# Kernel optimization log

Hardware: AMD Instinct MI355X
Metric: run time of the kernel (lower is better)

## Reference

```python
import jax, jax.numpy as jnp
import numpy as np

B, BT = 64, 16              # total crops, true batch (B = 4 crops * BT)
IMG, PATCH, C = 224, 16, 3
EMB, HEADS, DEPTH = 192, 3, 12
MLP = 4 * EMB
NPATCH = (IMG // PATCH) ** 2      # 196
NTOK = NPATCH + 1                 # 197 (cls + patches)
NSLICE = 16
SAT_H, SAT_DK = 8, 32             # ScaledDotProductAttention(d_model=192, d_k=d_v=32, h=8)
SAT_D = SAT_H * SAT_DK            # 256


def setup_inputs() -> dict:
    ks = jax.random.split(jax.random.key(0), 16)
    n = lambda i, shape: jax.random.normal(ks[i], shape, jnp.float32) * 0.02
    z = lambda *s: jnp.zeros(s, jnp.float32)
    o = lambda *s: jnp.ones(s, jnp.float32)
    return {
        "x": jax.random.normal(ks[0], (B, C, IMG, IMG), jnp.float32),
        "x_g_norm": jax.random.uniform(ks[1], (BT, 1, IMG, IMG), dtype=jnp.float32),
        "per_li": jnp.linspace(1.0 / 16.0, 15.0 / 16.0, 15, dtype=jnp.float32),
        "per_li_var": jnp.linspace(0.01, 0.15, 15, dtype=jnp.float32),
        "patch_w": n(2, (EMB, C, PATCH, PATCH)), "patch_b": z(EMB),
        "cls_token": n(3, (1, 1, EMB)), "pos_embed": n(4, (1, NTOK, EMB)),
        "eleva_embed": n(5, (NSLICE, EMB)), "eleva_var_embed": n(6, (NSLICE, EMB)),
        "sat_wq": n(7, (EMB, SAT_D)), "sat_bq": z(SAT_D),
        "sat_wk": n(8, (EMB, SAT_D)), "sat_bk": z(SAT_D),
        "sat_wv": n(9, (EMB, SAT_D)), "sat_bv": z(SAT_D),
        "sat_wo": n(10, (SAT_D, EMB)), "sat_bo": z(EMB),
        "ln1_w": o(DEPTH, EMB), "ln1_b": z(DEPTH, EMB),
        "qkv_w": n(11, (DEPTH, EMB, 3 * EMB)),
        "proj_w": n(12, (DEPTH, EMB, EMB)), "proj_b": z(DEPTH, EMB),
        "ln2_w": o(DEPTH, EMB), "ln2_b": z(DEPTH, EMB),
        "fc1_w": n(13, (DEPTH, EMB, MLP)), "fc1_b": z(DEPTH, MLP),
        "fc2_w": n(14, (DEPTH, MLP, EMB)), "fc2_b": z(DEPTH, EMB),
        "lnf_w": o(EMB), "lnf_b": z(EMB),
    }


def _ln(x, w, b, eps=1e-5):
    mu = x.mean(-1, keepdims=True)
    var = ((x - mu) ** 2).mean(-1, keepdims=True)
    return (x - mu) * jax.lax.rsqrt(var + eps) * w + b


def reference(x, x_g_norm, per_li, per_li_var, patch_w, patch_b, cls_token, pos_embed,
              eleva_embed, eleva_var_embed, sat_wq, sat_bq, sat_wk, sat_bk, sat_wv, sat_bv,
              sat_wo, sat_bo, ln1_w, ln1_b, qkv_w, proj_w, proj_b, ln2_w, ln2_b,
              fc1_w, fc1_b, fc2_w, fc2_b, lnf_w, lnf_b):
    Btot, Bt = x.shape[0], x_g_norm.shape[0]
    # --- PatchEmbed (Conv2d patch=stride=16) ---
    feat = jax.lax.conv_general_dilated(
        x, patch_w, (PATCH, PATCH), 'VALID',
        dimension_numbers=('NCHW', 'OIHW', 'NCHW')) + patch_b[None, :, None, None]
    tok = feat.reshape(Btot, EMB, NPATCH).transpose(0, 2, 1)          # [B,196,E]
    tok = jnp.concatenate([jnp.broadcast_to(cls_token, (Btot, 1, EMB)), tok], 1)
    tok = tok + pos_embed                                             # [B,197,E]
    # --- elevation indices (bisect_left on per-sample mean / unbiased var) ---
    flat = x_g_norm.reshape(Bt, -1)
    idx = jnp.searchsorted(per_li, flat.mean(-1), side='left')
    vidx = jnp.searchsorted(per_li_var, jnp.var(flat, axis=-1, ddof=1), side='left')
    crops = Btot // Bt
    ele = jnp.tile(eleva_embed[idx], (crops, 1))                      # [B,E]
    vele = jnp.tile(eleva_var_embed[vidx], (crops, 1))                # [B,E]
    # --- tiny 3-token attention per (sample, token), batched ---
    at = jnp.stack([tok,
                    jnp.broadcast_to(ele[:, None, :], tok.shape),
                    jnp.broadcast_to(vele[:, None, :], tok.shape)], axis=2)  # [B,T,3,E]
    M = Btot * NTOK
    at = at.reshape(M, 3, EMB)
    q = (at @ sat_wq + sat_bq).reshape(M, 3, SAT_H, SAT_DK).transpose(0, 2, 1, 3)
    k = (at @ sat_wk + sat_bk).reshape(M, 3, SAT_H, SAT_DK).transpose(0, 2, 1, 3)
    v = (at @ sat_wv + sat_bv).reshape(M, 3, SAT_H, SAT_DK).transpose(0, 2, 1, 3)
    att = jax.nn.softmax(jnp.einsum('mhqd,mhkd->mhqk', q, k) / np.sqrt(SAT_DK).astype(np.float32), axis=-1)
    o = jnp.einsum('mhqk,mhkd->mhqd', att, v).transpose(0, 2, 1, 3).reshape(M, 3, SAT_D)
    o = o @ sat_wo + sat_bo                                           # [M,3,E]
    tok = o.sum(1).reshape(Btot, NTOK, EMB)   # token' + eleEm' + elevarEm'
    # --- standard ViT blocks ---
    hd = EMB // HEADS
    scale = hd ** -0.5
    for i in range(DEPTH):
        h = _ln(tok, ln1_w[i], ln1_b[i])
        qkv = (h @ qkv_w[i]).reshape(Btot, NTOK, 3, HEADS, hd).transpose(2, 0, 3, 1, 4)
        a = jax.nn.softmax(jnp.einsum('bhqd,bhkd->bhqk', qkv[0], qkv[1]) * scale, axis=-1)
        h = jnp.einsum('bhqk,bhkd->bhqd', a, qkv[2]).transpose(0, 2, 1, 3).reshape(Btot, NTOK, EMB)
        tok = tok + h @ proj_w[i] + proj_b[i]
        h2 = _ln(tok, ln2_w[i], ln2_b[i])
        h2 = jax.nn.gelu(h2 @ fc1_w[i] + fc1_b[i], approximate=False)
        tok = tok + h2 @ fc2_w[i] + fc2_b[i]
    tok = _ln(tok, lnf_w, lnf_b)
    return tok[:, 0]
```

## Files before the change

### kernel.cpp

```cpp
#include <hip/hip_runtime.h>
#include <hip/hip_bf16.h>
#include <math.h>

#define NB 64
#define NBT 16
#define IMG 224
#define CIN 3
#define EMB 192
#define NHEADS 3
#define DEPTH 12
#define MLPD (4*EMB)
#define NPATCH 196
#define NTOK 197
#define M_TOK (NB*NTOK)
#define M_PATCH (NB*NPATCH)
#define SAT_H 8
#define SAT_DK 32
#define SAT_D 256
#define KPV 232

typedef __attribute__((ext_vector_type(8))) short bf16x8;
typedef __attribute__((ext_vector_type(4))) float f32x4;
typedef __hip_bfloat16 bf16;

__device__ __forceinline__ float bf2f(ushort u) { return __uint_as_float(((unsigned)u) << 16); }
__device__ __forceinline__ ushort f2bf(float f) {
    bf16 h = __float2bfloat16(f);
    return *reinterpret_cast<ushort*>(&h);
}

__global__ __launch_bounds__(256) void stats_kernel(const float* __restrict__ xg,
    const float* __restrict__ per_li, const float* __restrict__ per_li_var,
    int* __restrict__ idx_out)
{
    int s = blockIdx.x;
    const float* row = xg + (size_t)s * (IMG*IMG);
    double lsum = 0.0, lsq = 0.0;
    for (int i = threadIdx.x; i < IMG*IMG; i += 256) {
        double v = (double)row[i]; lsum += v; lsq += v*v;
    }
    __shared__ double ssum[256], ssq[256];
    ssum[threadIdx.x] = lsum; ssq[threadIdx.x] = lsq;
    __syncthreads();
    for (int st = 128; st > 0; st >>= 1) {
        if (threadIdx.x < st) { ssum[threadIdx.x] += ssum[threadIdx.x+st]; ssq[threadIdx.x] += ssq[threadIdx.x+st]; }
        __syncthreads();
    }
    if (threadIdx.x == 0) {
        double n = (double)(IMG*IMG);
        double mean = ssum[0] / n;
        double var  = (ssq[0] - n*mean*mean) / (n - 1.0);
        int i1 = 0, i2 = 0;
        for (int j = 0; j < 15; j++) {
            if ((double)per_li[j] < mean) i1++;
            if ((double)per_li_var[j] < var) i2++;
        }
        idx_out[s] = i1; idx_out[16 + s] = i2;
    }
}

__global__ __launch_bounds__(256) void transpose_cast_kernel(const float* __restrict__ in,
    bf16* __restrict__ out, int K, int N)
{
    in  += (size_t)blockIdx.z*K*N;
    out += (size_t)blockIdx.z*N*K;
    __shared__ float t[32][33];
    int k0 = blockIdx.y*32, n0 = blockIdx.x*32;
    int tx = threadIdx.x & 31, ty = threadIdx.x >> 5;
    #pragma unroll
    for (int i = 0; i < 4; i++) {
        int k = ty + i*8;
        t[k][tx] = in[(size_t)(k0+k)*N + n0 + tx];
    }
    __syncthreads();
    #pragma unroll
    for (int i = 0; i < 4; i++) {
        int n = ty + i*8;
        out[(size_t)(n0+n)*K + k0 + tx] = __float2bfloat16(t[tx][n]);
    }
}

__global__ __launch_bounds__(256) void cast_kernel(const float* __restrict__ in, bf16* __restrict__ out, int n)
{
    int i = blockIdx.x*256 + threadIdx.x;
    if (i < n) out[i] = __float2bfloat16(in[i]);
}

__global__ __launch_bounds__(256) void im2col_kernel(const float* __restrict__ x, bf16* __restrict__ out)
{
    int e = blockIdx.x*256 + threadIdx.x;
    if (e >= M_PATCH*768) return;
    int row = e / 768, col = e % 768;
    int b = row / NPATCH, p = row % NPATCH;
    int py = p / 14, px = p % 14;
    int c = col >> 8, r8 = col & 255;
    int i = r8 >> 4, j = r8 & 15;
    out[e] = __float2bfloat16(x[(((size_t)b*CIN + c)*IMG + py*16 + i)*IMG + px*16 + j]);
}

__global__ void cls_kernel(const float* __restrict__ cls, const float* __restrict__ pos, bf16* __restrict__ tokb)
{
    int i = blockIdx.x*256 + threadIdx.x;
    if (i >= NB*EMB) return;
    int b = i / EMB, e = i % EMB;
    tokb[(size_t)(b*NTOK)*EMB + e] = __float2bfloat16(cls[e] + pos[e]);
}

template<int EPI, bool OBF>
__global__ __launch_bounds__(256) void mfma_gemm(
    const bf16* __restrict__ A, const bf16* __restrict__ Wt,
    const float* __restrict__ bias, const float* __restrict__ aux,
    void* __restrict__ Cv, int M, int N, int K, int ldc, float bias_scale)
{
    __shared__ bf16 As[64][72];
    __shared__ bf16 Bs[64][72];
    int tid = threadIdx.x;
    int wave = tid >> 6, lane = tid & 63;
    int wm = wave >> 1, wn = wave & 1;
    int m0 = blockIdx.y*64, n0 = blockIdx.x*64;
    f32x4 acc[2][2] = {};
    int sr = tid >> 3, sc = (tid & 7) * 8;

    for (int k0 = 0; k0 < K; k0 += 64) {
        #pragma unroll
        for (int it = 0; it < 2; it++) {
            int r = sr + it*32;
            *(uint4*)&As[r][sc] = *(const uint4*)(A  + (size_t)(m0 + r)*K + k0 + sc);
            *(uint4*)&Bs[r][sc] = *(const uint4*)(Wt + (size_t)(n0 + r)*K + k0 + sc);
        }
        __syncthreads();
        #pragma unroll
        for (int ks = 0; ks < 2; ks++) {
            int ko = ks*32 + (lane >> 4)*8;
            bf16x8 af[2], bfr[2];
            #pragma unroll
            for (int mi = 0; mi < 2; mi++) af[mi]  = *(const bf16x8*)&As[wm*32 + mi*16 + (lane & 15)][ko];
            #pragma unroll
            for (int ni = 0; ni < 2; ni++) bfr[ni] = *(const bf16x8*)&Bs[wn*32 + ni*16 + (lane & 15)][ko];
            #pragma unroll
            for (int mi = 0; mi < 2; mi++)
                #pragma unroll
                for (int ni = 0; ni < 2; ni++)
                    acc[mi][ni] = __builtin_amdgcn_mfma_f32_16x16x32_bf16(af[mi], bfr[ni], acc[mi][ni], 0, 0, 0);
        }
        __syncthreads();
    }
    #pragma unroll
    for (int mi = 0; mi < 2; mi++) {
        #pragma unroll
        for (int ni = 0; ni < 2; ni++) {
            int rbase = m0 + wm*32 + mi*16 + (lane >> 4)*4;
            int col   = n0 + wn*32 + ni*16 + (lane & 15);
            #pragma unroll
            for (int r = 0; r < 4; r++) {
                int row = rbase + r;
                float v = acc[mi][ni][r];
                if constexpr (EPI == 4) {
                    int b_ = row / NPATCH, p = row % NPATCH;
                    ((bf16*)Cv)[(size_t)(b_*NTOK + 1 + p)*EMB + col] =
                        __float2bfloat16(v + bias[col] + aux[(size_t)(1+p)*EMB + col]);
                } else if constexpr (EPI == 5) {
                    int hd = row >> 6, d = row & 63;
                    int bb = col / NTOK, t = col - bb*NTOK;
                    ((bf16*)Cv)[((size_t)((bb*3 + hd)*64 + d))*KPV + t] = __float2bfloat16(v);
                } else {
                    if constexpr (EPI == 1) v += bias[col]*bias_scale;
                    if constexpr (EPI == 2) v = ((float*)Cv)[(size_t)row*ldc + col] + v + bias[col];
                    if constexpr (EPI == 3) { v += bias[col]; v = 0.5f*v*(1.0f + erff(v*0.70710678118654752f)); }
                    if constexpr (OBF) ((bf16*)Cv)[(size_t)row*ldc + col] = __float2bfloat16(v);
                    else               ((float*)Cv)[(size_t)row*ldc + col] = v;
                }
            }
        }
    }
}

__global__ __launch_bounds__(256) void sat_rows_kernel(
    const float* __restrict__ eleva, const float* __restrict__ eleva_var,
    const float* __restrict__ wq, const float* __restrict__ bq,
    const float* __restrict__ wk, const float* __restrict__ bk,
    const float* __restrict__ wv, const float* __restrict__ bv,
    const int* __restrict__ idx, float* __restrict__ proj, float* __restrict__ sconst)
{
    int s = blockIdx.x;
    __shared__ float ev[2][EMB];
    __shared__ float pr[6][SAT_D];
    int t = threadIdx.x;
    for (int i = t; i < 2*EMB; i += 256) {
        if (i < EMB) ev[0][i] = eleva[(size_t)idx[s]*EMB + i];
        else         ev[1][i-EMB] = eleva_var[(size_t)idx[16+s]*EMB + (i-EMB)];
    }
    __syncthreads();
    for (int j = 0; j < 6; j++) {
        const float* vec = ev[(j >= 3) ? 1 : 0];
        const float* Wm = (j%3 == 0) ? wq : ((j%3 == 1) ? wk : wv);
        const float* bm = (j%3 == 0) ? bq : ((j%3 == 1) ? bk : bv);
        float accv = bm[t];
        for (int k = 0; k < EMB; k++) accv += vec[k]*Wm[(size_t)k*SAT_D + t];
        pr[j][t] = accv;
        proj[((size_t)s*6 + j)*SAT_D + t] = accv;
    }
    __syncthreads();
    if (t < 32) {
        int h = t >> 2, c = t & 3;
        const float* qv = pr[(c < 2) ? 0 : 3];
        const float* kv = pr[((c & 1) == 0) ? 1 : 4];
        float d = 0.f;
        for (int x = 0; x < SAT_DK; x++) d += qv[h*32+x]*kv[h*32+x];
        sconst[((size_t)s*8 + h)*4 + c] = d * 0.17677669529663687f;
    }
}

__global__ __launch_bounds__(256) void sat_attn_kernel(
    const bf16* __restrict__ qkv0, const float* __restrict__ proj,
    const float* __restrict__ sconst, bf16* __restrict__ osum)
{
    int b = blockIdx.x;
    int s = b & 15;
    __shared__ float pr[6][SAT_D];
    __shared__ float sc[8][4];
    for (int i = threadIdx.x; i < 6*SAT_D; i += 256) pr[i >> 8][i & 255] = proj[(size_t)s*6*SAT_D + i];
    if (threadIdx.x < 32) sc[threadIdx.x >> 2][threadIdx.x & 3] = sconst[(size_t)s*32 + threadIdx.x];
    __syncthreads();
    int t = threadIdx.x;
    if (t >= NTOK) return;
    size_t m = (size_t)b*NTOK + t;
    const ushort* q0 = (const ushort*)(qkv0 + m*768);
    const ushort* k0 = q0 + 256;
    const ushort* v0 = q0 + 512;
    const float inv = 0.17677669529663687f;
    for (int h = 0; h < SAT_H; h++) {
        int d0 = h*32;
        float S00=0,S01=0,S02=0,S10=0,S20=0;
        #pragma unroll 8
        for (int d = 0; d < 32; d++) {
            float qv = bf2f(q0[d0+d]), kv = bf2f(k0[d0+d]);
            S00 += qv*kv;
            S01 += qv*pr[1][d0+d];
            S02 += qv*pr[4][d0+d];
            S10 += pr[0][d0+d]*kv;
            S20 += pr[3][d0+d]*kv;
        }
        S00*=inv; S01*=inv; S02*=inv; S10*=inv; S20*=inv;
        float al=0.f, be=0.f, ga=0.f;
        {
            float mx = fmaxf(S00, fmaxf(S01, S02));
            float e0 = expf(S00-mx), e1 = expf(S01-mx), e2 = expf(S02-mx);
            float is = 1.0f/(e0+e1+e2); al += e0*is; be += e1*is; ga += e2*is;
        }
        {
            float a1 = sc[h][0], a2 = sc[h][1];
            float mx = fmaxf(S10, fmaxf(a1, a2));
            float e0 = expf(S10-mx), e1 = expf(a1-mx), e2 = expf(a2-mx);
            float is = 1.0f/(e0+e1+e2); al += e0*is; be += e1*is; ga += e2*is;
        }
        {
            float a1 = sc[h][2], a2 = sc[h][3];
            float mx = fmaxf(S20, fmaxf(a1, a2));
            float e0 = expf(S20-mx), e1 = expf(a1-mx), e2 = expf(a2-mx);
            float is = 1.0f/(e0+e1+e2); al += e0*is; be += e1*is; ga += e2*is;
        }
        #pragma unroll 8
        for (int d = 0; d < 32; d++)
            osum[m*SAT_D + d0 + d] = __float2bfloat16(al*bf2f(v0[d0+d]) + be*pr[2][d0+d] + ga*pr[5][d0+d]);
    }
}

__global__ __launch_bounds__(256) void vit_attn_mfma(
    const bf16* __restrict__ qkv, const bf16* __restrict__ vT, bf16* __restrict__ hout)
{
    __shared__ ushort Ks[208*72];
    __shared__ ushort Vt[64*KPV];
    __shared__ ushort Pl[4][16*KPV];

    int u = (blockIdx.x & 7)*96 + (blockIdx.x >> 3);
    int qg = u & 3, hd = (u >> 2) % 3, b = u / 12;
    int tid = threadIdx.x;
    size_t rowQ = (size_t)b*NTOK;

    for (int i = tid; i < 208*8; i += 256) {
        int k = i >> 3, c = i & 7;
        uint4 v = make_uint4(0u,0u,0u,0u);
        if (k < NTOK) v = *(const uint4*)(qkv + (rowQ + k)*384 + 192 + hd*64 + c*8);
        *(uint4*)&Ks[(size_t)k*72 + c*8] = v;
    }
    {
        const uint4* vsrc = (const uint4*)(vT + (size_t)((b*3 + hd)*64)*KPV);
        uint4* vdst = (uint4*)Vt;
        for (int i = tid; i < 64*KPV/8; i += 256) vdst[i] = vsrc[i];
    }
    __syncthreads();

    int wave = tid >> 6, lane = tid & 63;
    int qstart = (13*qg + 3) >> 2;
    int qcnt   = ((13*(qg+1) + 3) >> 2) - qstart;
    if (wave >= qcnt) return;
    int q0 = (qstart + wave)*16;
    int qcol = lane & 15, g = lane >> 4;

    bf16x8 qf[2] = {};
    if (q0 + qcol < NTOK) {
        const bf16* qp = qkv + (rowQ + q0 + qcol)*384 + hd*64 + g*8;
        qf[0] = *(const bf16x8*)qp;
        qf[1] = *(const bf16x8*)(qp + 32);
    }

    f32x4 st[13] = {};
    #pragma unroll
    for (int t = 0; t < 13; t++) {
        const ushort* krow = &Ks[(size_t)(16*t + qcol)*72];
        bf16x8 a0 = *(const bf16x8*)(krow + g*8);
        bf16x8 a1 = *(const bf16x8*)(krow + 32 + g*8);
        st[t] = __builtin_amdgcn_mfma_f32_16x16x32_bf16(a0, qf[0], st[t], 0, 0, 0);
        st[t] = __builtin_amdgcn_mfma_f32_16x16x32_bf16(a1, qf[1], st[t], 0, 0, 0);
    }

    const float scale = 0.125f;
    float mx = -1e30f;
    #pragma unroll
    for (int t = 0; t < 13; t++)
        #pragma unroll
        for (int r = 0; r < 4; r++) {
            int key = 16*t + 4*g + r;
            float s = st[t][r]*scale;
            st[t][r] = s;
            if (key < NTOK) mx = fmaxf(mx, s);
        }
    mx = fmaxf(mx, __shfl_xor(mx, 16));
    mx = fmaxf(mx, __shfl_xor(mx, 32));
    float sum = 0.f;
    #pragma unroll
    for (int t = 0; t < 13; t++)
        #pragma unroll
        for (int r = 0; r < 4; r++) {
            int key = 16*t + 4*g + r;
            float e = (key < NTOK) ? __expf(st[t][r] - mx) : 0.f;
            st[t][r] = e; sum += e;
        }
    sum += __shfl_xor(sum, 16);
    sum += __shfl_xor(sum, 32);
    float isv = 1.f/sum;

    ushort* P = Pl[wave];
    #pragma unroll
    for (int t = 0; t < 13; t++)
        #pragma unroll
        for (int r = 0; r < 4; r++)
            P[(size_t)qcol*KPV + 16*t + 4*g + r] = f2bf(st[t][r]*isv);
    #pragma unroll
    for (int r = 0; r < 4; r++)
        P[(size_t)qcol*KPV + 208 + 4*g + r] = 0;

    f32x4 oacc[4] = {};
    #pragma unroll
    for (int ks = 0; ks < 7; ks++) {
        bf16x8 pf = *(const bf16x8*)&P[(size_t)qcol*KPV + ks*32 + g*8];
        #pragma unroll
        for (int dt = 0; dt < 4; dt++) {
            bf16x8 vf = *(const bf16x8*)&Vt[(size_t)(dt*16 + qcol)*KPV + ks*32 + g*8];
            oacc[dt] = __builtin_amdgcn_mfma_f32_16x16x32_bf16(pf, vf, oacc[dt], 0, 0, 0);
        }
    }

    int nq = NTOK - q0; if (nq > 16) nq = 16;
    #pragma unroll
    for (int dt = 0; dt < 4; dt++)
        #pragma unroll
        for (int r = 0; r < 4; r++) {
            int q = 4*g + r;
            if (q < nq)
                hout[(rowQ + q0 + q)*EMB + hd*64 + dt*16 + qcol] = __float2bfloat16(oacc[dt][r]);
        }
}

__global__ __launch_bounds__(256) void ln_kernel(const float* __restrict__ in,
    const float* __restrict__ w, const float* __restrict__ b_, bf16* __restrict__ out, int nrows)
{
    int r = blockIdx.x*4 + (threadIdx.x >> 6);
    int lane = threadIdx.x & 63;
    if (r >= nrows) return;
    const float* x = in + (size_t)r*EMB;
    float x0 = x[lane], x1 = x[lane+64], x2 = x[lane+128];
    float s = x0+x1+x2;
    for (int o = 32; o > 0; o >>= 1) s += __shfl_xor(s, o);
    float mu = s * (1.0f/EMB);
    float d0 = x0-mu, d1 = x1-mu, d2 = x2-mu;
    float ss = d0*d0 + d1*d1 + d2*d2;
    for (int o = 32; o > 0; o >>= 1) ss += __shfl_xor(ss, o);
    float rs = rsqrtf(ss*(1.0f/EMB) + 1e-5f);
    bf16* y = out + (size_t)r*EMB;
    y[lane]     = __float2bfloat16(d0*rs*w[lane]     + b_[lane]);
    y[lane+64]  = __float2bfloat16(d1*rs*w[lane+64]  + b_[lane+64]);
    y[lane+128] = __float2bfloat16(d2*rs*w[lane+128] + b_[lane+128]);
}

__global__ __launch_bounds__(64) void final_ln_kernel(const float* __restrict__ tok,
    const float* __restrict__ w, const float* __restrict__ b_, float* __restrict__ out)
{
    int b = blockIdx.x, lane = threadIdx.x;
    const float* x = tok + (size_t)b*NTOK*EMB;
    float x0 = x[lane], x1 = x[lane+64], x2 = x[lane+128];
    float s = x0+x1+x2;
    for (int o = 32; o > 0; o >>= 1) s += __shfl_xor(s, o);
    float mu = s * (1.0f/EMB);
    float d0 = x0-mu, d1 = x1-mu, d2 = x2-mu;
    float ss = d0*d0 + d1*d1 + d2*d2;
    for (int o = 32; o > 0; o >>= 1) ss += __shfl_xor(ss, o);
    float rs = rsqrtf(ss*(1.0f/EMB) + 1e-5f);
    out[(size_t)b*EMB + lane]     = d0*rs*w[lane]     + b_[lane];
    out[(size_t)b*EMB + lane+64]  = d1*rs*w[lane+64]  + b_[lane+64];
    out[(size_t)b*EMB + lane+128] = d2*rs*w[lane+128] + b_[lane+128];
}

extern "C" void kernel_launch(void* const* d_in, const int* in_sizes, int n_in,
                              void* d_out, int out_size, void* d_ws, size_t ws_size,
                              hipStream_t stream)
{
    const float* x          = (const float*)d_in[0];
    const float* xg         = (const float*)d_in[1];
    const float* per_li     = (const float*)d_in[2];
    const float* per_li_var = (const float*)d_in[3];
    const float* patch_w    = (const float*)d_in[4];
    const float* patch_b    = (const float*)d_in[5];
    const float* cls_token  = (const float*)d_in[6];
    const float* pos_embed  = (const float*)d_in[7];
    const float* eleva      = (const float*)d_in[8];
    const float* eleva_var  = (const float*)d_in[9];
    const float* sat_wq     = (const float*)d_in[10];
    const float* sat_bq     = (const float*)d_in[11];
    const float* sat_wk     = (const float*)d_in[12];
    const float* sat_bk     = (const float*)d_in[13];
    const float* sat_wv     = (const float*)d_in[14];
    const float* sat_bv     = (const float*)d_in[15];
    const float* sat_wo     = (const float*)d_in[16];
    const float* sat_bo     = (const float*)d_in[17];
    const float* ln1_w      = (const float*)d_in[18];
    const float* ln1_b      = (const float*)d_in[19];
    const float* qkv_w      = (const float*)d_in[20];
    const float* proj_w     = (const float*)d_in[21];
    const float* proj_b     = (const float*)d_in[22];
    const float* ln2_w      = (const float*)d_in[23];
    const float* ln2_b      = (const float*)d_in[24];
    const float* fc1_w      = (const float*)d_in[25];
    const float* fc1_b      = (const float*)d_in[26];
    const float* fc2_w      = (const float*)d_in[27];
    const float* fc2_b      = (const float*)d_in[28];
    const float* lnf_w      = (const float*)d_in[29];
    const float* lnf_b      = (const float*)d_in[30];
    float* out = (float*)d_out;

    char* p = (char*)d_ws;
    float* tokf = (float*)p;                 p += (size_t)M_TOK*EMB*4;
    bf16* hb    = (bf16*)p;                  p += (size_t)M_TOK*EMB*2;
    bf16* tokb  = (bf16*)p;                  p += (size_t)M_TOK*EMB*2;
    bf16* qkvb  = (bf16*)p;                  p += (size_t)M_TOK*768*2;
    bf16* osum  = (bf16*)p;                  p += (size_t)M_TOK*SAT_D*2;
    bf16* vTb   = (bf16*)p;                  p += (size_t)NB*3*64*KPV*2;
    bf16* qkv_wt  = (bf16*)p;                p += (size_t)DEPTH*576*EMB*2;
    bf16* proj_wt = (bf16*)p;                p += (size_t)DEPTH*EMB*EMB*2;
    bf16* fc1_wt  = (bf16*)p;                p += (size_t)DEPTH*MLPD*EMB*2;
    bf16* fc2_wt  = (bf16*)p;                p += (size_t)DEPTH*EMB*MLPD*2;
    bf16* patch_wb= (bf16*)p;                p += (size_t)EMB*768*2;
    bf16* sat_wqt = (bf16*)p;                p += (size_t)SAT_D*EMB*2;
    bf16* sat_wkt = (bf16*)p;                p += (size_t)SAT_D*EMB*2;
    bf16* sat_wvt = (bf16*)p;                p += (size_t)SAT_D*EMB*2;
    bf16* sat_wot = (bf16*)p;                p += (size_t)EMB*SAT_D*2;
    float* projb  = (float*)p;               p += 16*6*SAT_D*4;
    float* sconst = (float*)p;               p += 16*32*4;
    int*   idxb   = (int*)p;

    transpose_cast_kernel<<<dim3(576/32, EMB/32, DEPTH), 256, 0, stream>>>(qkv_w,  qkv_wt,  EMB, 576);
    transpose_cast_kernel<<<dim3(EMB/32, EMB/32, DEPTH), 256, 0, stream>>>(proj_w, proj_wt, EMB, EMB);
    transpose_cast_kernel<<<dim3(MLPD/32, EMB/32, DEPTH), 256, 0, stream>>>(fc1_w, fc1_wt,  EMB, MLPD);
    transpose_cast_kernel<<<dim3(EMB/32, MLPD/32, DEPTH), 256, 0, stream>>>(fc2_w, fc2_wt,  MLPD, EMB);
    transpose_cast_kernel<<<dim3(SAT_D/32, EMB/32, 1), 256, 0, stream>>>(sat_wq, sat_wqt, EMB, SAT_D);
    transpose_cast_kernel<<<dim3(SAT_D/32, EMB/32, 1), 256, 0, stream>>>(sat_wk, sat_wkt, EMB, SAT_D);
    transpose_cast_kernel<<<dim3(SAT_D/32, EMB/32, 1), 256, 0, stream>>>(sat_wv, sat_wvt, EMB, SAT_D);
    transpose_cast_kernel<<<dim3(EMB/32, SAT_D/32, 1), 256, 0, stream>>>(sat_wo, sat_wot, SAT_D, EMB);
    cast_kernel<<<(EMB*768 + 255)/256, 256, 0, stream>>>(patch_w, patch_wb, EMB*768);

    stats_kernel<<<16, 256, 0, stream>>>(xg, per_li, per_li_var, idxb);
    im2col_kernel<<<(M_PATCH*768 + 255)/256, 256, 0, stream>>>(x, qkvb);
    mfma_gemm<4,true><<<dim3(EMB/64, M_PATCH/64), 256, 0, stream>>>(
        qkvb, patch_wb, patch_b, pos_embed, tokb, M_PATCH, EMB, 768, EMB, 1.0f);
    cls_kernel<<<(NB*EMB + 255)/256, 256, 0, stream>>>(cls_token, pos_embed, tokb);
    sat_rows_kernel<<<16, 256, 0, stream>>>(eleva, eleva_var, sat_wq, sat_bq, sat_wk, sat_bk,
                                            sat_wv, sat_bv, idxb, projb, sconst);
    mfma_gemm<1,true><<<dim3(SAT_D/64, M_TOK/64), 256, 0, stream>>>(
        tokb, sat_wqt, sat_bq, nullptr, qkvb + 0,   M_TOK, SAT_D, EMB, 768, 1.0f);
    mfma_gemm<1,true><<<dim3(SAT_D/64, M_TOK/64), 256, 0, stream>>>(
        tokb, sat_wkt, sat_bk, nullptr, qkvb + 256, M_TOK, SAT_D, EMB, 768, 1.0f);
    mfma_gemm<1,true><<<dim3(SAT_D/64, M_TOK/64), 256, 0, stream>>>(
        tokb, sat_wvt, sat_bv, nullptr, qkvb + 512, M_TOK, SAT_D, EMB, 768, 1.0f);
    sat_attn_kernel<<<NB, 256, 0, stream>>>(qkvb, projb, sconst, osum);
    mfma_gemm<1,false><<<dim3(EMB/64, M_TOK/64), 256, 0, stream>>>(
        osum, sat_wot, sat_bo, nullptr, tokf, M_TOK, EMB, SAT_D, EMB, 3.0f);
    for (int i = 0; i < DEPTH; i++) {
        ln_kernel<<<M_TOK/4, 256, 0, stream>>>(tokf, ln1_w + i*EMB, ln1_b + i*EMB, hb, M_TOK);
        mfma_gemm<0,true><<<dim3(384/64, M_TOK/64), 256, 0, stream>>>(
            hb, qkv_wt + (size_t)i*576*EMB, nullptr, nullptr, qkvb, M_TOK, 384, EMB, 384, 1.0f);
        mfma_gemm<5,true><<<dim3(M_TOK/64, EMB/64), 256, 0, stream>>>(
            qkv_wt + ((size_t)i*576 + 384)*EMB, hb, nullptr, nullptr, vTb, EMB, M_TOK, EMB, 0, 1.0f);
        vit_attn_mfma<<<768, 256, 0, stream>>>(qkvb, vTb, hb);
        mfma_gemm<2,false><<<dim3(EMB/64, M_TOK/64), 256, 0, stream>>>(
            hb, proj_wt + (size_t)i*EMB*EMB, proj_b + i*EMB, nullptr, tokf, M_TOK, EMB, EMB, EMB, 1.0f);
        ln_kernel<<<M_TOK/4, 256, 0, stream>>>(tokf, ln2_w + i*EMB, ln2_b + i*EMB, hb, M_TOK);
        mfma_gemm<3,true><<<dim3(MLPD/64, M_TOK/64), 256, 0, stream>>>(
            hb, fc1_wt + (size_t)i*MLPD*EMB, fc1_b + i*MLPD, nullptr, qkvb, M_TOK, MLPD, EMB, MLPD, 1.0f);
        mfma_gemm<2,false><<<dim3(EMB/64, M_TOK/64), 256, 0, stream>>>(
            qkvb, fc2_wt + (size_t)i*EMB*MLPD, fc2_b + i*EMB, nullptr, tokf, M_TOK, EMB, MLPD, EMB, 1.0f);
    }
    final_ln_kernel<<<NB, 64, 0, stream>>>(tokf, lnf_w, lnf_b, out);
}
```

Measured before the change: 1.636 ms.

## Fuse LayerNorm into full-row GEMM epilogues, merge SAT QKV GEMMs, split stats

```diff
diff --git a/kernel.cpp b/kernel.cpp
--- a/kernel.cpp
+++ b/kernel.cpp
@@ -29,34 +29,46 @@
     return *reinterpret_cast<ushort*>(&h);
 }
 
-__global__ __launch_bounds__(256) void stats_kernel(const float* __restrict__ xg,
-    const float* __restrict__ per_li, const float* __restrict__ per_li_var,
-    int* __restrict__ idx_out)
-{
-    int s = blockIdx.x;
-    const float* row = xg + (size_t)s * (IMG*IMG);
-    double lsum = 0.0, lsq = 0.0;
-    for (int i = threadIdx.x; i < IMG*IMG; i += 256) {
-        double v = (double)row[i]; lsum += v; lsq += v*v;
+__global__ __launch_bounds__(256) void stats1_kernel(const float* __restrict__ xg, double* __restrict__ part)
+{
+    int j = blockIdx.x, s = blockIdx.y;
+    const float4* src = (const float4*)(xg + (size_t)s*(IMG*IMG)) + (size_t)j*784;
+    double ls = 0.0, lq = 0.0;
+    for (int i = threadIdx.x; i < 784; i += 256) {
+        float4 v = src[i];
+        double a = v.x, b = v.y, c = v.z, d = v.w;
+        ls += a+b+c+d;
+        lq += a*a + b*b + c*c + d*d;
     }
     __shared__ double ssum[256], ssq[256];
-    ssum[threadIdx.x] = lsum; ssq[threadIdx.x] = lsq;
+    ssum[threadIdx.x] = ls; ssq[threadIdx.x] = lq;
     __syncthreads();
     for (int st = 128; st > 0; st >>= 1) {
         if (threadIdx.x < st) { ssum[threadIdx.x] += ssum[threadIdx.x+st]; ssq[threadIdx.x] += ssq[threadIdx.x+st]; }
         __syncthreads();
     }
     if (threadIdx.x == 0) {
-        double n = (double)(IMG*IMG);
-        double mean = ssum[0] / n;
-        double var  = (ssq[0] - n*mean*mean) / (n - 1.0);
-        int i1 = 0, i2 = 0;
-        for (int j = 0; j < 15; j++) {
-            if ((double)per_li[j] < mean) i1++;
-            if ((double)per_li_var[j] < var) i2++;
-        }
-        idx_out[s] = i1; idx_out[16 + s] = i2;
-    }
+        part[(size_t)(s*16 + j)*2]     = ssum[0];
+        part[(size_t)(s*16 + j)*2 + 1] = ssq[0];
+    }
+}
+
+__global__ __launch_bounds__(64) void stats2_kernel(const double* __restrict__ part,
+    const float* __restrict__ per_li, const float* __restrict__ per_li_var, int* __restrict__ idx_out)
+{
+    int s = blockIdx.x;
+    if (threadIdx.x != 0) return;
+    double sum = 0.0, sq = 0.0;
+    for (int j = 0; j < 16; j++) { sum += part[(size_t)(s*16+j)*2]; sq += part[(size_t)(s*16+j)*2+1]; }
+    double n = (double)(IMG*IMG);
+    double mean = sum / n;
+    double var  = (sq - n*mean*mean) / (n - 1.0);
+    int i1 = 0, i2 = 0;
+    for (int j = 0; j < 15; j++) {
+        if ((double)per_li[j] < mean) i1++;
+        if ((double)per_li_var[j] < var) i2++;
+    }
+    idx_out[s] = i1; idx_out[16 + s] = i2;
 }
 
 __global__ __launch_bounds__(256) void transpose_cast_kernel(const float* __restrict__ in,
@@ -84,6 +96,15 @@
 {
     int i = blockIdx.x*256 + threadIdx.x;
     if (i < n) out[i] = __float2bfloat16(in[i]);
+}
+
+__global__ __launch_bounds__(256) void concat3_kernel(const float* __restrict__ a,
+    const float* __restrict__ b, const float* __restrict__ c, float* __restrict__ o)
+{
+    int i = blockIdx.x*256 + threadIdx.x;
+    if (i < 256) o[i] = a[i];
+    else if (i < 512) o[i] = b[i-256];
+    else if (i < 768) o[i] = c[i-512];
 }
 
 __global__ __launch_bounds__(256) void im2col_kernel(const float* __restrict__ x, bf16* __restrict__ out)
@@ -171,6 +192,73 @@
                     else               ((float*)Cv)[(size_t)row*ldc + col] = v;
                 }
             }
+        }
+    }
+}
+
+template<bool RESID>
+__global__ __launch_bounds__(256) void mfma_gemm_ln(
+    const bf16* __restrict__ A, const bf16* __restrict__ Wt,
+    const float* __restrict__ bias, float bias_scale,
+    const float* __restrict__ lnw, const float* __restrict__ lnb,
+    float* __restrict__ tokf, bf16* __restrict__ hbB, int K)
+{
+    __shared__ bf16 As[64][72];
+    __shared__ bf16 Bs[192][72];
+    __shared__ float sB[192], sW[192], sLb[192];
+    int tid = threadIdx.x;
+    int m0 = blockIdx.x*64;
+    if (tid < 192) { sB[tid] = bias[tid]*bias_scale; sW[tid] = lnw[tid]; sLb[tid] = lnb[tid]; }
+    int wave = tid >> 6, lane = tid & 63;
+    int qc = lane & 15, g = lane >> 4;
+    f32x4 acc[12] = {};
+    int sr = tid >> 3, sc = (tid & 7)*8;
+
+    for (int k0 = 0; k0 < K; k0 += 64) {
+        #pragma unroll
+        for (int it = 0; it < 2; it++)
+            *(uint4*)&As[sr + it*32][sc] = *(const uint4*)(A + (size_t)(m0 + sr + it*32)*K + k0 + sc);
+        #pragma unroll
+        for (int it = 0; it < 6; it++)
+            *(uint4*)&Bs[sr + it*32][sc] = *(const uint4*)(Wt + (size_t)(sr + it*32)*K + k0 + sc);
+        __syncthreads();
+        #pragma unroll
+        for (int ks = 0; ks < 2; ks++) {
+            bf16x8 af = *(const bf16x8*)&As[wave*16 + qc][ks*32 + g*8];
+            #pragma unroll
+            for (int c = 0; c < 12; c++) {
+                bf16x8 bf_ = *(const bf16x8*)&Bs[c*16 + qc][ks*32 + g*8];
+                acc[c] = __builtin_amdgcn_mfma_f32_16x16x32_bf16(af, bf_, acc[c], 0, 0, 0);
+            }
+        }
+        __syncthreads();
+    }
+    #pragma unroll
+    for (int r = 0; r < 4; r++) {
+        int row = m0 + wave*16 + g*4 + r;
+        float v[12];
+        float s = 0.f;
+        #pragma unroll
+        for (int c = 0; c < 12; c++) {
+            int col = c*16 + qc;
+            float t = acc[c][r] + sB[col];
+            if constexpr (RESID) t += tokf[(size_t)row*EMB + col];
+            v[c] = t; s += t;
+        }
+        #pragma unroll
+        for (int o = 1; o < 16; o <<= 1) s += __shfl_xor(s, o);
+        float mu = s * (1.0f/EMB);
+        float ss = 0.f;
+        #pragma unroll
+        for (int c = 0; c < 12; c++) { float d = v[c]-mu; ss += d*d; }
+        #pragma unroll
+        for (int o = 1; o < 16; o <<= 1) ss += __shfl_xor(ss, o);
+        float rsn = rsqrtf(ss*(1.0f/EMB) + 1e-5f);
+        #pragma unroll
+        for (int c = 0; c < 12; c++) {
+            int col = c*16 + qc;
+            tokf[(size_t)row*EMB + col] = v[c];
+            hbB[(size_t)row*EMB + col] = __float2bfloat16((v[c]-mu)*rsn*sW[col] + sLb[col]);
         }
     }
 }
@@ -371,27 +459,6 @@
             if (q < nq)
                 hout[(rowQ + q0 + q)*EMB + hd*64 + dt*16 + qcol] = __float2bfloat16(oacc[dt][r]);
         }
-}
-
-__global__ __launch_bounds__(256) void ln_kernel(const float* __restrict__ in,
-    const float* __restrict__ w, const float* __restrict__ b_, bf16* __restrict__ out, int nrows)
-{
-    int r = blockIdx.x*4 + (threadIdx.x >> 6);
-    int lane = threadIdx.x & 63;
-    if (r >= nrows) return;
-    const float* x = in + (size_t)r*EMB;
-    float x0 = x[lane], x1 = x[lane+64], x2 = x[lane+128];
-    float s = x0+x1+x2;
-    for (int o = 32; o > 0; o >>= 1) s += __shfl_xor(s, o);
-    float mu = s * (1.0f/EMB);
-    float d0 = x0-mu, d1 = x1-mu, d2 = x2-mu;
-    float ss = d0*d0 + d1*d1 + d2*d2;
-    for (int o = 32; o > 0; o >>= 1) ss += __shfl_xor(ss, o);
-    float rs = rsqrtf(ss*(1.0f/EMB) + 1e-5f);
-    bf16* y = out + (size_t)r*EMB;
-    y[lane]     = __float2bfloat16(d0*rs*w[lane]     + b_[lane]);
-    y[lane+64]  = __float2bfloat16(d1*rs*w[lane+64]  + b_[lane+64]);
-    y[lane+128] = __float2bfloat16(d2*rs*w[lane+128] + b_[lane+128]);
 }
 
 __global__ __launch_bounds__(64) void final_ln_kernel(const float* __restrict__ tok,
@@ -461,54 +528,57 @@
     bf16* fc1_wt  = (bf16*)p;                p += (size_t)DEPTH*MLPD*EMB*2;
     bf16* fc2_wt  = (bf16*)p;                p += (size_t)DEPTH*EMB*MLPD*2;
     bf16* patch_wb= (bf16*)p;                p += (size_t)EMB*768*2;
-    bf16* sat_wqt = (bf16*)p;                p += (size_t)SAT_D*EMB*2;
-    bf16* sat_wkt = (bf16*)p;                p += (size_t)SAT_D*EMB*2;
-    bf16* sat_wvt = (bf16*)p;                p += (size_t)SAT_D*EMB*2;
+    bf16* sat_wqkvt = (bf16*)p;              p += (size_t)3*SAT_D*EMB*2;
     bf16* sat_wot = (bf16*)p;                p += (size_t)EMB*SAT_D*2;
+    float* sat_bqkv = (float*)p;             p += 768*4;
     float* projb  = (float*)p;               p += 16*6*SAT_D*4;
     float* sconst = (float*)p;               p += 16*32*4;
+    double* statp = (double*)p;              p += 256*2*8;
     int*   idxb   = (int*)p;
 
     transpose_cast_kernel<<<dim3(576/32, EMB/32, DEPTH), 256, 0, stream>>>(qkv_w,  qkv_wt,  EMB, 576);
     transpose_cast_kernel<<<dim3(EMB/32, EMB/32, DEPTH), 256, 0, stream>>>(proj_w, proj_wt, EMB, EMB);
     transpose_cast_kernel<<<dim3(MLPD/32, EMB/32, DEPTH), 256, 0, stream>>>(fc1_w, fc1_wt,  EMB, MLPD);
     transpose_cast_kernel<<<dim3(EMB/32, MLPD/32, DEPTH), 256, 0, stream>>>(fc2_w, fc2_wt,  MLPD, EMB);
-    transpose_cast_kernel<<<dim3(SAT_D/32, EMB/32, 1), 256, 0, stream>>>(sat_wq, sat_wqt, EMB, SAT_D);
-    transpose_cast_kernel<<<dim3(SAT_D/32, EMB/32, 1), 256, 0, stream>>>(sat_wk, sat_wkt, EMB, SAT_D);
-    transpose_cast_kernel<<<dim3(SAT_D/32, EMB/32, 1), 256, 0, stream>>>(sat_wv, sat_wvt, EMB, SAT_D);
+    transpose_cast_kernel<<<dim3(SAT_D/32, EMB/32, 1), 256, 0, stream>>>(sat_wq, sat_wqkvt,              EMB, SAT_D);
+    transpose_cast_kernel<<<dim3(SAT_D/32, EMB/32, 1), 256, 0, stream>>>(sat_wk, sat_wqkvt + 256*EMB,    EMB, SAT_D);
+    transpose_cast_kernel<<<dim3(SAT_D/32, EMB/32, 1), 256, 0, stream>>>(sat_wv, sat_wqkvt + 512*EMB,    EMB, SAT_D);
     transpose_cast_kernel<<<dim3(EMB/32, SAT_D/32, 1), 256, 0, stream>>>(sat_wo, sat_wot, SAT_D, EMB);
+    concat3_kernel<<<3, 256, 0, stream>>>(sat_bq, sat_bk, sat_bv, sat_bqkv);
     cast_kernel<<<(EMB*768 + 255)/256, 256, 0, stream>>>(patch_w, patch_wb, EMB*768);
 
-    stats_kernel<<<16, 256, 0, stream>>>(xg, per_li, per_li_var, idxb);
+    stats1_kernel<<<dim3(16, 16), 256, 0, stream>>>(xg, statp);
+    stats2_kernel<<<16, 64, 0, stream>>>(statp, per_li, per_li_var, idxb);
     im2col_kernel<<<(M_PATCH*768 + 255)/256, 256, 0, stream>>>(x, qkvb);
     mfma_gemm<4,true><<<dim3(EMB/64, M_PATCH/64), 256, 0, stream>>>(
         qkvb, patch_wb, patch_b, pos_embed, tokb, M_PATCH, EMB, 768, EMB, 1.0f);
     cls_kernel<<<(NB*EMB + 255)/256, 256, 0, stream>>>(cls_token, pos_embed, tokb);
     sat_rows_kernel<<<16, 256, 0, stream>>>(eleva, eleva_var, sat_wq, sat_bq, sat_wk, sat_bk,
                                             sat_wv, sat_bv, idxb, projb, sconst);
-    mfma_gemm<1,true><<<dim3(SAT_D/64, M_TOK/64), 256, 0, stream>>>(
-        tokb, sat_wqt, sat_bq, nullptr, qkvb + 0,   M_TOK, SAT_D, EMB, 768, 1.0f);
-    mfma_gemm<1,true><<<dim3(SAT_D/64, M_TOK/64), 256, 0, stream>>>(
-        tokb, sat_wkt, sat_bk, nullptr, qkvb + 256, M_TOK, SAT_D, EMB, 768, 1.0f);
-    mfma_gemm<1,true><<<dim3(SAT_D/64, M_TOK/64), 256, 0, stream>>>(
-        tokb, sat_wvt, sat_bv, nullptr, qkvb + 512, M_TOK, SAT_D, EMB, 768, 1.0f);
+    mfma_gemm<1,true><<<dim3(768/64, M_TOK/64), 256, 0, stream>>>(
+        tokb, sat_wqkvt, sat_bqkv, nullptr, qkvb, M_TOK, 768, EMB, 768, 1.0f);
     sat_attn_kernel<<<NB, 256, 0, stream>>>(qkvb, projb, sconst, osum);
-    mfma_gemm<1,false><<<dim3(EMB/64, M_TOK/64), 256, 0, stream>>>(
-        osum, sat_wot, sat_bo, nullptr, tokf, M_TOK, EMB, SAT_D, EMB, 3.0f);
+    mfma_gemm_ln<false><<<M_TOK/64, 256, 0, stream>>>(
+        osum, sat_wot, sat_bo, 3.0f, ln1_w, ln1_b, tokf, hb, SAT_D);
     for (int i = 0; i < DEPTH; i++) {
-        ln_kernel<<<M_TOK/4, 256, 0, stream>>>(tokf, ln1_w + i*EMB, ln1_b + i*EMB, hb, M_TOK);
         mfma_gemm<0,true><<<dim3(384/64, M_TOK/64), 256, 0, stream>>>(
             hb, qkv_wt + (size_t)i*576*EMB, nullptr, nullptr, qkvb, M_TOK, 384, EMB, 384, 1.0f);
         mfma_gemm<5,true><<<dim3(M_TOK/64, EMB/64), 256, 0, stream>>>(
             qkv_wt + ((size_t)i*576 + 384)*EMB, hb, nullptr, nullptr, vTb, EMB, M_TOK, EMB, 0, 1.0f);
         vit_attn_mfma<<<768, 256, 0, stream>>>(qkvb, vTb, hb);
-        mfma_gemm<2,false><<<dim3(EMB/64, M_TOK/64), 256, 0, stream>>>(
-            hb, proj_wt + (size_t)i*EMB*EMB, proj_b + i*EMB, nullptr, tokf, M_TOK, EMB, EMB, EMB, 1.0f);
-        ln_kernel<<<M_TOK/4, 256, 0, stream>>>(tokf, ln2_w + i*EMB, ln2_b + i*EMB, hb, M_TOK);
+        mfma_gemm_ln<true><<<M_TOK/64, 256, 0, stream>>>(
+            hb, proj_wt + (size_t)i*EMB*EMB, proj_b + i*EMB, 1.0f,
+            ln2_w + i*EMB, ln2_b + i*EMB, tokf, hb, EMB);
         mfma_gemm<3,true><<<dim3(MLPD/64, M_TOK/64), 256, 0, stream>>>(
             hb, fc1_wt + (size_t)i*MLPD*EMB, fc1_b + i*MLPD, nullptr, qkvb, M_TOK, MLPD, EMB, MLPD, 1.0f);
-        mfma_gemm<2,false><<<dim3(EMB/64, M_TOK/64), 256, 0, stream>>>(
-            qkvb, fc2_wt + (size_t)i*EMB*MLPD, fc2_b + i*EMB, nullptr, tokf, M_TOK, EMB, MLPD, EMB, 1.0f);
+        if (i < DEPTH-1) {
+            mfma_gemm_ln<true><<<M_TOK/64, 256, 0, stream>>>(
+                qkvb, fc2_wt + (size_t)i*EMB*MLPD, fc2_b + i*EMB, 1.0f,
+                ln1_w + (i+1)*EMB, ln1_b + (i+1)*EMB, tokf, hb, MLPD);
+        } else {
+            mfma_gemm<2,false><<<dim3(EMB/64, M_TOK/64), 256, 0, stream>>>(
+                qkvb, fc2_wt + (size_t)i*EMB*MLPD, fc2_b + i*EMB, nullptr, tokf, M_TOK, EMB, MLPD, EMB, 1.0f);
+        }
     }
     final_ln_kernel<<<NB, 64, 0, stream>>>(tokf, lnf_w, lnf_b, out);
 }
```

Result: slower. 1.728 ms (+5.6%).
